# Kernel tuning notes

Hardware: AMD Instinct MI355X
Metric: run time of the kernel (lower is better)

Reference implementation:

```python
import jax, jax.numpy as jnp
import numpy as np

B, N, S, K = 8, 4096, 256, 128   # clouds, points/cloud, FPS samples (num_vote_test), neighbor cap
R = 0.2                           # ball-query radius
M = 45                            # FoldingNet grid side -> 45*45 = 2025 grid points


def _fps(pos):
    """Deterministic farthest point sampling of S points from pos [N,3] (start at index 0)."""
    n = pos.shape[0]
    big = jnp.finfo(pos.dtype).max

    def step(carry, _):
        mind, last = carry
        d = jnp.sum((pos - pos[last]) ** 2, axis=-1)
        mind = jnp.minimum(mind, d)
        nxt = jnp.argmax(mind).astype(jnp.int32)
        return (mind, nxt), nxt

    init = (jnp.full((n,), big, pos.dtype), jnp.int32(0))
    _, rest = jax.lax.scan(step, init, None, length=S - 1)
    return jnp.concatenate([jnp.zeros((1,), jnp.int32), rest])


def _forward(pos, Wt, bt, Wc1, bc1, Wc2, bc2, Wc3, bc3, We1, be1, We2, be2,
             Wf11, bf11, Wf12, bf12, Wf13, bf13, Wf21, bf21, Wf22, bf22, Wf23, bf23):
    lrelu = jax.nn.leaky_relu  # slope 0.01, matches torch LeakyReLU default
    # transformer: mlp([3,64]) -- BatchNorm at eval with default stats is identity
    x = lrelu(pos @ Wt + bt)                                  # [B,N,64]
    # FPS per cloud
    idx = jax.vmap(_fps)(pos)                                  # [B,S]
    new_pos = jnp.take_along_axis(pos, idx[..., None], axis=1)  # [B,S,3]
    # radius ball query: first K in-ball neighbors by index order (torch_cluster semantics)
    d2 = jnp.sum((new_pos[:, :, None, :] - pos[:, None, :, :]) ** 2, -1)  # [B,S,N]
    inball = d2 <= R * R
    keep = inball & (jnp.cumsum(inball, axis=-1) <= K)
    order = jnp.where(keep, jnp.arange(N)[None, None, :], N)
    nidx = jnp.sort(order, axis=-1)[..., :K]                   # [B,S,K]
    valid = nidx < N
    nsafe = jnp.minimum(nidx, N - 1)
    gather = jax.vmap(lambda a, i: a[i])
    xj = gather(x, nsafe)                                      # [B,S,K,64]
    pj = gather(pos, nsafe)                                    # [B,S,K,3]
    # PointConv: mlp(cat[x_j, pos_j - pos_i]) with max aggregation
    feat = jnp.concatenate([xj, pj - new_pos[:, :, None, :]], -1)  # [B,S,K,67]
    h = lrelu(feat @ Wc1 + bc1)
    h = lrelu(h @ Wc2 + bc2)
    h = lrelu(h @ Wc3 + bc3)                                   # [B,S,K,512]
    neg = jnp.finfo(h.dtype).min
    agg = jnp.max(jnp.where(valid[..., None], h, neg), axis=2)  # [B,S,512]
    # encoder mlp([515, 512, 2*bottleneck], last=True)
    e = lrelu(jnp.concatenate([agg, new_pos], -1) @ We1 + be1)
    e = e @ We2 + be2                                          # [B,S,2*bottleneck]
    mean, logvar = jnp.split(e, 2, axis=-1)
    std = jnp.exp(0.5 * logvar)
    # feature_selection (eval, rand=False): all S votes contribute; vote aggregation
    z = jnp.sum(mean / std, axis=1) / jnp.sum(1.0 / std, axis=1)  # [B,bottleneck]
    # FoldingNet decoder: 45x45 grid in [-0.3,0.3]^2, conv1x1 == last-dim linear
    g1 = np.linspace(-0.3, 0.3, M, dtype=np.float32)
    mg = np.meshgrid(g1, g1)
    grid = jnp.asarray(np.stack([mg[0].reshape(-1), mg[1].reshape(-1)], -1))  # [M*M,2]
    G = M * M
    code = jnp.broadcast_to(z[:, None, :], (z.shape[0], G, z.shape[1]))
    gb = jnp.broadcast_to(grid[None], (z.shape[0], G, 2))
    f = jnp.concatenate([code, gb], -1)                        # [B,G,bottleneck+2]
    f = jax.nn.relu(f @ Wf11 + bf11)
    f = jax.nn.relu(f @ Wf12 + bf12)
    f = f @ Wf13 + bf13                                        # [B,G,3]
    f2 = jnp.concatenate([code, f], -1)                        # [B,G,bottleneck+3]
    f2 = jax.nn.relu(f2 @ Wf21 + bf21)
    f2 = jax.nn.relu(f2 @ Wf22 + bf22)
    return f2 @ Wf23 + bf23                                    # [B,G,3]


_PARAM_SHAPES = [
    ("Wt", (3, 64)), ("bt", (64,)),
    ("Wc1", (67, 64)), ("bc1", (64,)),
    ("Wc2", (64, 128)), ("bc2", (128,)),
    ("Wc3", (128, 512)), ("bc3", (512,)),
    ("We1", (515, 512)), ("be1", (512,)),
    ("We2", (512, 2048)), ("be2", (2048,)),
    ("Wf11", (1026, 512)), ("bf11", (512,)),
    ("Wf12", (512, 512)), ("bf12", (512,)),
    ("Wf13", (512, 3)), ("bf13", (3,)),
    ("Wf21", (1027, 512)), ("bf21", (512,)),
    ("Wf22", (512, 512)), ("bf22", (512,)),
    ("Wf23", (512, 3)), ("bf23", (3,)),
]


def setup_inputs() -> dict:
    key = jax.random.key(0)
    inp = {"pos": jax.random.uniform(key, (B, N, 3), jnp.float32)}
    for i, (nm, sh) in enumerate(_PARAM_SHAPES):
        k = jax.random.fold_in(key, i + 1)
        fan_in = sh[0]
        inp[nm] = jax.random.normal(k, sh, jnp.float32) / np.sqrt(fan_in)
    return inp


def reference(pos, Wt, bt, Wc1, bc1, Wc2, bc2, Wc3, bc3, We1, be1, We2, be2,
              Wf11, bf11, Wf12, bf12, Wf13, bf13, Wf21, bf21, Wf22, bf22, Wf23, bf23):
    return _forward(pos, Wt, bt, Wc1, bc1, Wc2, bc2, Wc3, bc3, We1, be1, We2, be2,
                    Wf11, bf11, Wf12, bf12, Wf13, bf13, Wf21, bf21, Wf22, bf22, Wf23, bf23)
```

## Files before the change

kernel.cpp:

```cpp
#include <hip/hip_runtime.h>
#include <math.h>

#define BATCH 8
#define NPTS 4096
#define SSAMP 256
#define KNBR 128
#define GGRID 2025

typedef __attribute__((ext_vector_type(8))) short bf16x8;
typedef __attribute__((ext_vector_type(8))) unsigned short u16x8;
typedef __attribute__((ext_vector_type(4))) float f32x4;
#define MFMA16(a, b, c) __builtin_amdgcn_mfma_f32_16x16x32_bf16((a), (b), (c), 0, 0, 0)

__device__ __forceinline__ float lrelu01(float v) { return v > 0.f ? v : 0.01f * v; }
__device__ __forceinline__ unsigned short f2bf(float f) {
    unsigned u = __float_as_uint(f);
    unsigned r = (u + 0x7FFFu + ((u >> 16) & 1u)) >> 16;
    return (unsigned short)r;
}
__device__ __forceinline__ unsigned long long umax64(unsigned long long a, unsigned long long b) {
    return a > b ? a : b;
}
__device__ __forceinline__ void spin_ge(const int* p, int target) {
    while (__hip_atomic_load(p, __ATOMIC_RELAXED, __HIP_MEMORY_SCOPE_AGENT) < target)
        __builtin_amdgcn_s_sleep(16);
}
__device__ __forceinline__ float aload(const float* p) {
    return __hip_atomic_load((float*)p, __ATOMIC_RELAXED, __HIP_MEMORY_SCOPE_AGENT);
}
__device__ __forceinline__ void astore(float* p, float v) {
    __hip_atomic_store(p, v, __ATOMIC_RELAXED, __HIP_MEMORY_SCOPE_AGENT);
}

__global__ void preconv_kernel(const float* __restrict__ Wc1, const float* __restrict__ Wc2,
                               const float* __restrict__ Wc3, const float* __restrict__ We1,
                               const float* __restrict__ We2, const float* __restrict__ Wf12,
                               const float* __restrict__ Wf22,
                               unsigned short* __restrict__ W1T, unsigned short* __restrict__ W2T,
                               unsigned short* __restrict__ W3T, unsigned short* __restrict__ We1T,
                               unsigned short* __restrict__ We2T, unsigned short* __restrict__ Wf12T,
                               unsigned short* __restrict__ Wf22T) {
    int o = blockIdx.x * 256 + threadIdx.x;
    const int S1 = 6144, S2 = 8192, S3 = 65536, S4 = 294912, S5 = 1048576, S6 = 262144;
    if (o < S1) { int n = o / 96, k = o - n * 96; W1T[o] = f2bf(k < 67 ? Wc1[k * 64 + n] : 0.f); return; }
    o -= S1;
    if (o < S2) { int n = o >> 6, k = o & 63; W2T[o] = f2bf(Wc2[k * 128 + n]); return; }
    o -= S2;
    if (o < S3) { int n = o >> 7, k = o & 127; W3T[o] = f2bf(Wc3[k * 512 + n]); return; }
    o -= S3;
    if (o < S4) { int n = o / 576, k = o - n * 576; We1T[o] = f2bf(k < 515 ? We1[k * 512 + n] : 0.f); return; }
    o -= S4;
    if (o < S5) {
        int np = o >> 9, k = o & 511;
        int src = (np & 1) ? 1024 + (np >> 1) : (np >> 1);
        We2T[o] = f2bf(We2[(size_t)k * 2048 + src]);
        return;
    }
    o -= S5;
    if (o < S6) { int n = o >> 9, k = o & 511; Wf12T[o] = f2bf(Wf12[k * 512 + n]); return; }
    o -= S6;
    { int n = o >> 9, k = o & 511; Wf22T[o] = f2bf(Wf22[k * 512 + n]); }
}

__global__ void __launch_bounds__(256, 3) stage1_kernel(
    const float* __restrict__ pos, float* __restrict__ newpos, int* __restrict__ prog,
    const float* __restrict__ Wt, const float* __restrict__ bt,
    const unsigned short* __restrict__ W1T, const unsigned short* __restrict__ W2T,
    const unsigned short* __restrict__ W3T,
    const float* __restrict__ bc1, const float* __restrict__ bc2, const float* __restrict__ bc3,
    unsigned short* __restrict__ encin) {
    __shared__ __align__(16) unsigned char smem[53760];
    int blk = blockIdx.x, t = threadIdx.x;
    int wave = t >> 6, lane = t & 63;

    if (blk < 8) {
        float* pxs = (float*)smem;
        float* pys = (float*)(smem + 16384);
        float* pzs = (float*)(smem + 32768);
        float* npb = (float*)(smem + 49152);
        unsigned long long* rk = (unsigned long long*)(smem + 52224);
        int b = blk;
        const float* P = pos + (size_t)b * NPTS * 3;
        float* np = newpos + (size_t)b * SSAMP * 3;
        float px[16], py[16], pz[16], mind[16];
#pragma unroll
        for (int j = 0; j < 16; ++j) {
            int n = t + 256 * j;
            float X = P[n * 3 + 0], Y = P[n * 3 + 1], Z = P[n * 3 + 2];
            px[j] = X; py[j] = Y; pz[j] = Z;
            pxs[n] = X; pys[n] = Y; pzs[n] = Z;
            mind[j] = 3.402823466e+38f;
        }
        float cx = P[0], cy = P[1], cz = P[2];
        if (t == 0) { npb[0] = cx; npb[1] = cy; npb[2] = cz; }
        __syncthreads();
        for (int s = 1; s < SSAMP; ++s) {
            int p = s & 1;
            unsigned long long k[16];
#pragma unroll
            for (int j = 0; j < 16; ++j) {
                float dx = __fsub_rn(px[j], cx), dy = __fsub_rn(py[j], cy), dz = __fsub_rn(pz[j], cz);
                float d = __fadd_rn(__fadd_rn(__fmul_rn(dx, dx), __fmul_rn(dy, dy)), __fmul_rn(dz, dz));
                mind[j] = fminf(mind[j], d);
                k[j] = ((unsigned long long)__float_as_uint(mind[j]) << 32)
                     | (unsigned)~(unsigned)(t + 256 * j);
            }
#pragma unroll
            for (int st = 8; st > 0; st >>= 1)
#pragma unroll
                for (int j = 0; j < st; ++j) k[j] = umax64(k[j], k[j + st]);
            unsigned long long key = k[0];
            {
                unsigned long long a = __shfl_xor(key, 1, 64);
                unsigned long long b2 = __shfl_xor(key, 2, 64);
                unsigned long long c = __shfl_xor(key, 3, 64);
                key = umax64(umax64(key, a), umax64(b2, c));
                a = __shfl_xor(key, 4, 64);
                b2 = __shfl_xor(key, 8, 64);
                c = __shfl_xor(key, 12, 64);
                key = umax64(umax64(key, a), umax64(b2, c));
                a = __shfl_xor(key, 16, 64);
                b2 = __shfl_xor(key, 32, 64);
                c = __shfl_xor(key, 48, 64);
                key = umax64(umax64(key, a), umax64(b2, c));
            }
            if (lane == 0) rk[p * 4 + wave] = key;
            __syncthreads();
            unsigned long long k0 = rk[p * 4 + 0], k1 = rk[p * 4 + 1];
            unsigned long long k2 = rk[p * 4 + 2], k3 = rk[p * 4 + 3];
            unsigned long long bk = umax64(umax64(k0, k1), umax64(k2, k3));
            int nx = (int)(~(unsigned)(bk & 0xFFFFFFFFull));
            cx = pxs[nx]; cy = pys[nx]; cz = pzs[nx];
            if (t == 0) {
                npb[s * 3 + 0] = cx;
                npb[s * 3 + 1] = cy;
                npb[s * 3 + 2] = cz;
            }
            if ((s & 7) == 7) {
                if (t < 24) astore(&np[(s - 7) * 3 + t], npb[(s - 7) * 3 + t]);
                if (t == 0 && s >= 15)
                    __hip_atomic_store(&prog[b], s - 8, __ATOMIC_RELAXED, __HIP_MEMORY_SCOPE_AGENT);
            }
        }
        __syncthreads();
        if (t == 0)
            __hip_atomic_store(&prog[b], 255, __ATOMIC_RELAXED, __HIP_MEMORY_SCOPE_AGENT);
        return;
    }

    unsigned short* featl = (unsigned short*)smem;
    unsigned short* h2    = (unsigned short*)smem;
    unsigned short* h1    = (unsigned short*)(smem + 34816);
    float* mred = (float*)(smem + 34816);
    int*   vld  = (int*)(smem + 53248);
    int*   wl   = (int*)smem;
    int*   cnt  = (int*)(smem + 2048);
    float* wtb  = (float*)(smem + 26624);

    int cons = blk - 8;
    int s = cons >> 3, b = cons & 7;
    int bs = b * 256 + s;
    int quad = lane >> 4, l16 = lane & 15;

    if (t == 0) spin_ge(&prog[b], s);
    __syncthreads();
    float q0 = aload(&newpos[(size_t)bs * 3 + 0]);
    float q1 = aload(&newpos[(size_t)bs * 3 + 1]);
    float q2 = aload(&newpos[(size_t)bs * 3 + 2]);

    const float* P = pos + (size_t)b * NPTS * 3;
    {
        int base = 0;
        for (int c = 0; c < 16 && base < KNBR; ++c) {
            int n = wave * 1024 + c * 64 + lane;
            float dx = __fsub_rn(P[n * 3 + 0], q0);
            float dy = __fsub_rn(P[n * 3 + 1], q1);
            float dz = __fsub_rn(P[n * 3 + 2], q2);
            float d2 = __fadd_rn(__fadd_rn(__fmul_rn(dx, dx), __fmul_rn(dy, dy)), __fmul_rn(dz, dz));
            bool in = (d2 <= 0.04f);
            unsigned long long mask = __ballot(in);
            if (in) {
                int p = base + __popcll(mask & ((1ull << lane) - 1ull));
                if (p < KNBR) wl[wave * 128 + p] = n;
            }
            base += __popcll(mask);
        }
        if (lane == 0) cnt[wave] = base < KNBR ? base : KNBR;
    }
    __syncthreads();
    {
        int c0 = cnt[0], c1 = cnt[1], c2 = cnt[2], c3 = cnt[3];
        if (t < 128) {
            int idx = -1, r = t;
            if (r < c0) idx = wl[r];
            else {
                r -= c0;
                if (r < c1) idx = wl[128 + r];
                else {
                    r -= c1;
                    if (r < c2) idx = wl[256 + r];
                    else { r -= c2; if (r < c3) idx = wl[384 + r]; }
                }
            }
            vld[t] = idx;
        }
        if (t < 192) wtb[t] = Wt[t];
        else wtb[t] = bt[t - 192];
    }
    __syncthreads();

    int vbits = 0;
#pragma unroll
    for (int i = 0; i < 2; ++i)
#pragma unroll
        for (int reg = 0; reg < 4; ++reg)
            if (vld[(2 * wave + i) * 16 + quad * 4 + reg] >= 0) vbits |= 1 << (i * 4 + reg);

    {
        int sr = t >> 1, sh = t & 1;
        int n = vld[sr];
        int ns = n < 0 ? 0 : n;
        const float* pp = pos + ((size_t)b * NPTS + ns) * 3;
        float p0 = pp[0], p1 = pp[1], p2 = pp[2];
        unsigned short* frow = &featl[sr * 104];
        u16x8 z8 = {0, 0, 0, 0, 0, 0, 0, 0};
        if (n >= 0) {
#pragma unroll
            for (int g = 0; g < 4; ++g) {
                u16x8 v8;
#pragma unroll
                for (int e = 0; e < 8; ++e) {
                    int c = sh * 32 + g * 8 + e;
                    float v = fmaf(p2, wtb[128 + c], fmaf(p1, wtb[64 + c], fmaf(p0, wtb[c], wtb[192 + c])));
                    v8[e] = (unsigned short)f2bf(lrelu01(v));
                }
                *(u16x8*)&frow[sh * 32 + g * 8] = v8;
            }
        } else {
#pragma unroll
            for (int g = 0; g < 4; ++g) *(u16x8*)&frow[sh * 32 + g * 8] = z8;
        }
        if (sh == 1) {
            u16x8 dv = z8;
            if (n >= 0) {
                dv[0] = (unsigned short)f2bf(__fsub_rn(p0, q0));
                dv[1] = (unsigned short)f2bf(__fsub_rn(p1, q1));
                dv[2] = (unsigned short)f2bf(__fsub_rn(p2, q2));
            }
            *(u16x8*)&frow[64] = dv;
            *(u16x8*)&frow[72] = z8;
            *(u16x8*)&frow[80] = z8;
            *(u16x8*)&frow[88] = z8;
        }
    }
    __syncthreads();

    {
        f32x4 acc[2][4];
#pragma unroll
        for (int i = 0; i < 2; ++i)
#pragma unroll
            for (int nt = 0; nt < 4; ++nt) acc[i][nt] = (f32x4){0.f, 0.f, 0.f, 0.f};
#pragma unroll
        for (int ks = 0; ks < 3; ++ks) {
            bf16x8 afr[2];
#pragma unroll
            for (int i = 0; i < 2; ++i)
                afr[i] = *(const bf16x8*)&featl[((2 * wave + i) * 16 + l16) * 104 + ks * 32 + quad * 8];
#pragma unroll
            for (int nt = 0; nt < 4; ++nt) {
                bf16x8 bfr = *(const bf16x8*)(W1T + (nt * 16 + l16) * 96 + ks * 32 + quad * 8);
                acc[0][nt] = MFMA16(afr[0], bfr, acc[0][nt]);
                acc[1][nt] = MFMA16(afr[1], bfr, acc[1][nt]);
            }
        }
#pragma unroll
        for (int i = 0; i < 2; ++i)
#pragma unroll
            for (int nt = 0; nt < 4; ++nt) {
                int col = nt * 16 + l16;
                float bias = bc1[col];
#pragma unroll
                for (int reg = 0; reg < 4; ++reg) {
                    int row = (2 * wave + i) * 16 + quad * 4 + reg;
                    h1[row * 72 + col] = f2bf(lrelu01(acc[i][nt][reg] + bias));
                }
            }
    }
    __syncthreads();

    {
        f32x4 acc[2][8];
#pragma unroll
        for (int i = 0; i < 2; ++i)
#pragma unroll
            for (int nt = 0; nt < 8; ++nt) acc[i][nt] = (f32x4){0.f, 0.f, 0.f, 0.f};
#pragma unroll
        for (int ks = 0; ks < 2; ++ks) {
            bf16x8 afr[2];
#pragma unroll
            for (int i = 0; i < 2; ++i)
                afr[i] = *(const bf16x8*)&h1[((2 * wave + i) * 16 + l16) * 72 + ks * 32 + quad * 8];
#pragma unroll
            for (int nt = 0; nt < 8; ++nt) {
                bf16x8 bfr = *(const bf16x8*)(W2T + (nt * 16 + l16) * 64 + ks * 32 + quad * 8);
                acc[0][nt] = MFMA16(afr[0], bfr, acc[0][nt]);
                acc[1][nt] = MFMA16(afr[1], bfr, acc[1][nt]);
            }
        }
        __syncthreads();
#pragma unroll
        for (int i = 0; i < 2; ++i)
#pragma unroll
            for (int nt = 0; nt < 8; ++nt) {
                int col = nt * 16 + l16;
                float bias = bc2[col];
#pragma unroll
                for (int reg = 0; reg < 4; ++reg) {
                    int row = (2 * wave + i) * 16 + quad * 4 + reg;
                    h2[row * 136 + col] = f2bf(lrelu01(acc[i][nt][reg] + bias));
                }
            }
    }
    __syncthreads();

    for (int c3 = 0; c3 < 4; ++c3) {
        f32x4 acc[2][8];
#pragma unroll
        for (int i = 0; i < 2; ++i)
#pragma unroll
            for (int nt = 0; nt < 8; ++nt) acc[i][nt] = (f32x4){0.f, 0.f, 0.f, 0.f};
#pragma unroll
        for (int ks = 0; ks < 4; ++ks) {
            bf16x8 afr[2];
#pragma unroll
            for (int i = 0; i < 2; ++i)
                afr[i] = *(const bf16x8*)&h2[((2 * wave + i) * 16 + l16) * 136 + ks * 32 + quad * 8];
#pragma unroll
            for (int nt = 0; nt < 8; ++nt) {
                bf16x8 bfr = *(const bf16x8*)(W3T + ((size_t)((c3 * 8 + nt) * 16 + l16)) * 128 + ks * 32 + quad * 8);
                acc[0][nt] = MFMA16(afr[0], bfr, acc[0][nt]);
                acc[1][nt] = MFMA16(afr[1], bfr, acc[1][nt]);
            }
        }
#pragma unroll
        for (int nt = 0; nt < 8; ++nt) {
            float vmax = -3.402823466e+38f;
#pragma unroll
            for (int i = 0; i < 2; ++i)
#pragma unroll
                for (int reg = 0; reg < 4; ++reg)
                    if (vbits & (1 << (i * 4 + reg))) vmax = fmaxf(vmax, acc[i][nt][reg]);
            vmax = fmaxf(vmax, __shfl_xor(vmax, 16));
            vmax = fmaxf(vmax, __shfl_xor(vmax, 32));
            if (lane < 16) mred[wave * 512 + (c3 * 8 + nt) * 16 + l16] = vmax;
        }
    }
    __syncthreads();
    unsigned short* erow = encin + (size_t)bs * 576;
    for (int c = t; c < 576; c += 256) {
        unsigned short v;
        if (c < 512) {
            float m4 = fmaxf(fmaxf(mred[c], mred[512 + c]), fmaxf(mred[1024 + c], mred[1536 + c]));
            v = f2bf(lrelu01(m4 + bc3[c]));
        } else if (c < 515) {
            v = f2bf(c == 512 ? q0 : (c == 513 ? q1 : q2));
        } else v = 0;
        erow[c] = v;
    }
}

__global__ void __launch_bounds__(256, 2) tail_kernel(
    const unsigned short* __restrict__ encinh, const unsigned short* __restrict__ We1T,
    const float* __restrict__ be1, unsigned short* __restrict__ e1h,
    const unsigned short* __restrict__ We2T, const float* __restrict__ be2,
    float* __restrict__ zacc, int* __restrict__ cnts,
    const float* __restrict__ Wf11, const float* __restrict__ bf11,
    const float* __restrict__ Wf21, const float* __restrict__ bf21,
    float* __restrict__ u1, float* __restrict__ u2,
    const unsigned short* __restrict__ Wf12T, const float* __restrict__ bf12,
    const float* __restrict__ Wf13, const float* __restrict__ bf13,
    const unsigned short* __restrict__ Wf22T, const float* __restrict__ bf22,
    const float* __restrict__ Wf23, const float* __restrict__ bf23,
    float* __restrict__ pts, float* __restrict__ outv) {
    __shared__ __align__(16) unsigned char smem[40960];
    int blk = blockIdx.x, t = threadIdx.x;
    int wave = t >> 6, lane = t & 63, quad = lane >> 4, l16 = lane & 15;

    if (blk < 320) {
        unsigned short* As = (unsigned short*)smem;
        bool is_e1 = blk < 64;
        int rb, cb;
        const unsigned short* A;
        const unsigned short* BT;
        int Ka;
        if (is_e1) { rb = blk >> 2; cb = blk & 3; A = encinh; BT = We1T; Ka = 576; }
        else {
            int j = blk - 64; rb = j >> 4; cb = j & 15; A = e1h; BT = We2T; Ka = 512;
            if (t == 0) spin_ge(&cnts[rb], 4);
            __syncthreads();
            __threadfence();
        }
        int row0 = rb * 128, col0 = cb * 128;
        f32x4 acc[2][8];
#pragma unroll
        for (int i = 0; i < 2; ++i)
#pragma unroll
            for (int nt = 0; nt < 8; ++nt) acc[i][nt] = (f32x4){0.f, 0.f, 0.f, 0.f};
        int nk = Ka >> 6;
        int sr = t >> 1, sh = t & 1;
        const unsigned short* Arow = A + (size_t)(row0 + sr) * Ka + sh * 32;
        for (int ks = 0; ks < nk; ++ks) {
            u16x8 av[4];
#pragma unroll
            for (int j = 0; j < 4; ++j) av[j] = *(const u16x8*)(Arow + ks * 64 + j * 8);
            __syncthreads();
#pragma unroll
            for (int j = 0; j < 4; ++j) *(u16x8*)&As[sr * 72 + sh * 32 + j * 8] = av[j];
            __syncthreads();
#pragma unroll
            for (int ks2 = 0; ks2 < 2; ++ks2) {
                bf16x8 afr0 = *(const bf16x8*)&As[((2 * wave) * 16 + l16) * 72 + ks2 * 32 + quad * 8];
                bf16x8 afr1 = *(const bf16x8*)&As[((2 * wave + 1) * 16 + l16) * 72 + ks2 * 32 + quad * 8];
#pragma unroll
                for (int nt = 0; nt < 8; ++nt) {
                    bf16x8 bfr = *(const bf16x8*)(BT + (size_t)(col0 + nt * 16 + l16) * Ka + ks * 64 + ks2 * 32 + quad * 8);
                    acc[0][nt] = MFMA16(afr0, bfr, acc[0][nt]);
                    acc[1][nt] = MFMA16(afr1, bfr, acc[1][nt]);
                }
            }
        }
        if (is_e1) {
#pragma unroll
            for (int i = 0; i < 2; ++i)
#pragma unroll
                for (int nt = 0; nt < 8; ++nt) {
                    int col = col0 + nt * 16 + l16;
                    float bv = be1[col];
#pragma unroll
                    for (int reg = 0; reg < 4; ++reg) {
                        int row = row0 + (2 * wave + i) * 16 + quad * 4 + reg;
                        e1h[(size_t)row * 512 + col] = f2bf(lrelu01(acc[i][nt][reg] + bv));
                    }
                }
            __syncthreads();
            if (t == 0) { __threadfence(); atomicAdd(&cnts[rb], 1); }
        } else {
            int b = row0 >> 8;
#pragma unroll
            for (int nt = 0; nt < 8; ++nt) {
                int colp = col0 + nt * 16 + l16;
                int c2 = colp >> 1;
                int srcc = (colp & 1) ? 1024 + c2 : c2;
                float bv = be2[srcc];
                float num = 0.f, den = 0.f;
#pragma unroll
                for (int i = 0; i < 2; ++i)
#pragma unroll
                    for (int reg = 0; reg < 4; ++reg) {
                        float val = acc[i][nt][reg] + bv;
                        float par = __shfl_xor(val, 1, 64);
                        float d = expf(-0.5f * par);
                        num += val * d;
                        den += d;
                    }
                num += __shfl_xor(num, 16, 64); den += __shfl_xor(den, 16, 64);
                num += __shfl_xor(num, 32, 64); den += __shfl_xor(den, 32, 64);
                if (quad == 0 && !(l16 & 1)) {
                    atomicAdd(&zacc[((b << 10) + c2) * 2 + 0], num);
                    atomicAdd(&zacc[((b << 10) + c2) * 2 + 1], den);
                }
            }
            __syncthreads();
            if (t == 0) atomicAdd(&cnts[16], 1);
        }
        return;
    }

    if (blk < 336) {
        float* zt = (float*)smem;
        float* red = (float*)(smem + 32768);
        int j = blk - 320;
        int dec = j >> 3, cb = j & 7;
        const float* W = dec ? Wf21 : Wf11;
        const float* bias = dec ? bf21 : bf11;
        float* u = dec ? u2 : u1;
        if (t == 0) spin_ge(&cnts[16], 256);
        __syncthreads();
#pragma unroll
        for (int i = 0; i < 32; ++i) {
            int o = t + i * 256;
            float num = aload(&zacc[o * 2 + 0]);
            float den = aload(&zacc[o * 2 + 1]);
            zt[(o & 1023) * 8 + (o >> 10)] = num / den;
        }
        __syncthreads();
        int c64 = t & 63, kc = t >> 6;
        int co = cb * 64 + c64;
        float acc[8];
#pragma unroll
        for (int r = 0; r < 8; ++r) acc[r] = 0.f;
        for (int i = 0; i < 256; ++i) {
            int ci = kc * 256 + i;
            float w = W[(size_t)ci * 512 + co];
            const float4* zp = (const float4*)&zt[ci * 8];
            float4 z0 = zp[0], z1 = zp[1];
            acc[0] = fmaf(z0.x, w, acc[0]); acc[1] = fmaf(z0.y, w, acc[1]);
            acc[2] = fmaf(z0.z, w, acc[2]); acc[3] = fmaf(z0.w, w, acc[3]);
            acc[4] = fmaf(z1.x, w, acc[4]); acc[5] = fmaf(z1.y, w, acc[5]);
            acc[6] = fmaf(z1.z, w, acc[6]); acc[7] = fmaf(z1.w, w, acc[7]);
        }
#pragma unroll
        for (int r = 0; r < 8; ++r) red[(kc * 64 + c64) * 8 + r] = acc[r];
        __syncthreads();
        if (kc == 0) {
#pragma unroll
            for (int r = 0; r < 8; ++r) {
                float v = red[(0 * 64 + c64) * 8 + r] + red[(1 * 64 + c64) * 8 + r]
                        + red[(2 * 64 + c64) * 8 + r] + red[(3 * 64 + c64) * 8 + r] + bias[co];
                astore(&u[r * 512 + co], v);
            }
        }
        __syncthreads();
        if (t == 0) atomicAdd(&cnts[17 + dec], 1);
        return;
    }

    {
        unsigned short* As = (unsigned short*)smem;
        float* sW = (float*)(smem + 18432);
        float* sU = (float*)(smem + 24576);
        float* sP = (float*)(smem + 28672);
        float* sB = (float*)(smem + 30208);
        float* sRC = (float*)(smem + 30720);
        int dec = blk < 844 ? 0 : 1;
        int idx0 = blk - (dec ? 844 : 336);
        int j = idx0 >> 2, cc = idx0 & 3;
        const float* u = dec ? u2 : u1;
        const float* Wfold = dec ? Wf21 : Wf11;
        int nExtra = dec ? 3 : 2;
        const unsigned short* WT = dec ? Wf22T : Wf12T;
        const float* bmid = dec ? bf22 : bf12;
        const float* wout = dec ? Wf23 : Wf13;
        const float* bout = dec ? bf23 : bf13;
        float* ov = dec ? outv : pts;
        int row0 = j * 128, col0 = cc * 128;
        int b0 = row0 / 2025;

        if (t == 0) {
            spin_ge(&cnts[17 + dec], 8);
            if (dec) spin_ge(&cnts[20 + j], 4);
        }
        __syncthreads();

        for (int idx = t; idx < 1536; idx += 256) {
            int r = idx >> 9, c = idx & 511;
            sW[r * 512 + c] = (r < nExtra) ? Wfold[(size_t)(1024 + r) * 512 + c] : 0.f;
        }
        for (int idx = t; idx < 1024; idx += 256) {
            int rb = idx >> 9;
            int bb = b0 + rb; if (bb > 7) bb = 7;
            sU[rb * 512 + (idx & 511)] = aload(&u[bb * 512 + (idx & 511)]);
        }
        for (int idx = t; idx < 384; idx += 256) sP[idx] = wout[col0 * 3 + idx];
        if (t < 128) sB[t] = bmid[col0 + t];
        if (t < 128) {
            int rg = row0 + t; if (rg > 16199) rg = 16199;
            int b = rg / 2025, g = rg - b * 2025;
            if (dec == 0) {
                int i = g / 45, jj = g - i * 45;
                sRC[t * 4 + 0] = (jj == 44) ? 0.3f : (float)(-0.3 + jj * (0.6 / 44.0));
                sRC[t * 4 + 1] = (i == 44) ? 0.3f : (float)(-0.3 + i * (0.6 / 44.0));
                sRC[t * 4 + 2] = 0.f;
            } else {
                sRC[t * 4 + 0] = aload(&pts[rg * 3 + 0]);
                sRC[t * 4 + 1] = aload(&pts[rg * 3 + 1]);
                sRC[t * 4 + 2] = aload(&pts[rg * 3 + 2]);
            }
            sRC[t * 4 + 3] = __int_as_float(b - b0);
        }
        __syncthreads();

        float proj[2][4][3];
#pragma unroll
        for (int i = 0; i < 2; ++i)
#pragma unroll
            for (int r = 0; r < 4; ++r) { proj[i][r][0] = 0.f; proj[i][r][1] = 0.f; proj[i][r][2] = 0.f; }

        int sr = t >> 1, sh = t & 1;
        float4 rc = *(const float4*)&sRC[sr * 4];
        int ubi = __float_as_int(rc.w);
        const float* up = sU + ubi * 512;
        f32x4 acc[2][8];
#pragma unroll
        for (int i = 0; i < 2; ++i)
#pragma unroll
            for (int nt = 0; nt < 8; ++nt) acc[i][nt] = (f32x4){0.f, 0.f, 0.f, 0.f};
        for (int ks = 0; ks < 8; ++ks) {
            __syncthreads();
            {
                int cbase = ks * 64 + sh * 32;
                const float4* w0p = (const float4*)&sW[cbase];
                const float4* w1p = (const float4*)&sW[512 + cbase];
                const float4* w2p = (const float4*)&sW[1024 + cbase];
                const float4* uup = (const float4*)&up[cbase];
#pragma unroll
                for (int g4 = 0; g4 < 8; ++g4) {
                    float4 w0 = w0p[g4], w1 = w1p[g4], w2 = w2p[g4], uu = uup[g4];
                    float v0 = fmaf(rc.z, w2.x, fmaf(rc.y, w1.x, fmaf(rc.x, w0.x, uu.x)));
                    float v1 = fmaf(rc.z, w2.y, fmaf(rc.y, w1.y, fmaf(rc.x, w0.y, uu.y)));
                    float v2 = fmaf(rc.z, w2.z, fmaf(rc.y, w1.z, fmaf(rc.x, w0.z, uu.z)));
                    float v3 = fmaf(rc.z, w2.w, fmaf(rc.y, w1.w, fmaf(rc.x, w0.w, uu.w)));
                    uint2 pk;
                    pk.x = (unsigned)f2bf(fmaxf(v0, 0.f)) | ((unsigned)f2bf(fmaxf(v1, 0.f)) << 16);
                    pk.y = (unsigned)f2bf(fmaxf(v2, 0.f)) | ((unsigned)f2bf(fmaxf(v3, 0.f)) << 16);
                    *(uint2*)&As[sr * 72 + sh * 32 + g4 * 4] = pk;
                }
            }
            __syncthreads();
#pragma unroll
            for (int ks2 = 0; ks2 < 2; ++ks2) {
                bf16x8 afr0 = *(const bf16x8*)&As[((2 * wave) * 16 + l16) * 72 + ks2 * 32 + quad * 8];
                bf16x8 afr1 = *(const bf16x8*)&As[((2 * wave + 1) * 16 + l16) * 72 + ks2 * 32 + quad * 8];
#pragma unroll
                for (int nt = 0; nt < 8; ++nt) {
                    bf16x8 bfr = *(const bf16x8*)(WT + (size_t)(col0 + nt * 16 + l16) * 512 + ks * 64 + ks2 * 32 + quad * 8);
                    acc[0][nt] = MFMA16(afr0, bfr, acc[0][nt]);
                    acc[1][nt] = MFMA16(afr1, bfr, acc[1][nt]);
                }
            }
        }
#pragma unroll
        for (int i = 0; i < 2; ++i)
#pragma unroll
            for (int nt = 0; nt < 8; ++nt) {
                int lc = nt * 16 + l16;
                float bv = sB[lc];
                float w0 = sP[lc * 3 + 0], w1 = sP[lc * 3 + 1], w2 = sP[lc * 3 + 2];
#pragma unroll
                for (int reg = 0; reg < 4; ++reg) {
                    float h = fmaxf(acc[i][nt][reg] + bv, 0.f);
                    proj[i][reg][0] = fmaf(h, w0, proj[i][reg][0]);
                    proj[i][reg][1] = fmaf(h, w1, proj[i][reg][1]);
                    proj[i][reg][2] = fmaf(h, w2, proj[i][reg][2]);
                }
            }
        float o0 = (cc == 0) ? bout[0] : 0.f;
        float o1 = (cc == 0) ? bout[1] : 0.f;
        float o2 = (cc == 0) ? bout[2] : 0.f;
#pragma unroll
        for (int i = 0; i < 2; ++i)
#pragma unroll
            for (int reg = 0; reg < 4; ++reg) {
                float p0 = proj[i][reg][0], p1 = proj[i][reg][1], p2 = proj[i][reg][2];
#pragma unroll
                for (int m = 1; m < 16; m <<= 1) {
                    p0 += __shfl_xor(p0, m, 64);
                    p1 += __shfl_xor(p1, m, 64);
                    p2 += __shfl_xor(p2, m, 64);
                }
                if (l16 == 0) {
                    int row = row0 + (2 * wave + i) * 16 + quad * 4 + reg;
                    if (row < 16200) {
                        atomicAdd(&ov[row * 3 + 0], p0 + o0);
                        atomicAdd(&ov[row * 3 + 1], p1 + o1);
                        atomicAdd(&ov[row * 3 + 2], p2 + o2);
                    }
                }
            }
        if (dec == 0) {
            __syncthreads();
            if (t == 0) atomicAdd(&cnts[20 + j], 1);
        }
    }
}

extern "C" void kernel_launch(void* const* d_in, const int* in_sizes, int n_in,
                              void* d_out, int out_size, void* d_ws, size_t ws_size,
                              hipStream_t stream) {
    const float* pos  = (const float*)d_in[0];
    const float* Wt   = (const float*)d_in[1];
    const float* bt   = (const float*)d_in[2];
    const float* Wc1  = (const float*)d_in[3];
    const float* bc1  = (const float*)d_in[4];
    const float* Wc2  = (const float*)d_in[5];
    const float* bc2  = (const float*)d_in[6];
    const float* Wc3  = (const float*)d_in[7];
    const float* bc3  = (const float*)d_in[8];
    const float* We1  = (const float*)d_in[9];
    const float* be1  = (const float*)d_in[10];
    const float* We2  = (const float*)d_in[11];
    const float* be2  = (const float*)d_in[12];
    const float* Wf11 = (const float*)d_in[13];
    const float* bf11 = (const float*)d_in[14];
    const float* Wf12 = (const float*)d_in[15];
    const float* bf12 = (const float*)d_in[16];
    const float* Wf13 = (const float*)d_in[17];
    const float* bf13 = (const float*)d_in[18];
    const float* Wf21 = (const float*)d_in[19];
    const float* bf21 = (const float*)d_in[20];
    const float* Wf22 = (const float*)d_in[21];
    const float* bf22 = (const float*)d_in[22];
    const float* Wf23 = (const float*)d_in[23];
    const float* bf23 = (const float*)d_in[24];
    float* out = (float*)d_out;

    float* wsf = (float*)d_ws;
    size_t off = 0;
    unsigned short* encinh= (unsigned short*)(wsf + off); off += 589824;
    unsigned short* e1h   = (unsigned short*)(wsf + off); off += 524288;
    float* zacc = wsf + off; off += 16384;
    float* u1   = wsf + off; off += 4096;
    float* u2   = wsf + off; off += 4096;
    float* pts  = wsf + off; off += 48600;
    float* newp = wsf + off; off += 6144;
    int*   prog = (int*)(wsf + off); off += 16;
    int*   cnts = (int*)(wsf + off); off += 256;
    unsigned short* W1T   = (unsigned short*)(wsf + off); off += 3072;
    unsigned short* W2T   = (unsigned short*)(wsf + off); off += 4096;
    unsigned short* W3T   = (unsigned short*)(wsf + off); off += 32768;
    unsigned short* We1T  = (unsigned short*)(wsf + off); off += 147456;
    unsigned short* We2T  = (unsigned short*)(wsf + off); off += 524288;
    unsigned short* Wf12T = (unsigned short*)(wsf + off); off += 131072;
    unsigned short* Wf22T = (unsigned short*)(wsf + off); off += 131072;

    hipMemsetAsync(prog, 0xFF, 64, stream);
    hipMemsetAsync(cnts, 0x00, 1024, stream);
    hipMemsetAsync(zacc, 0x00, 16384 * 4, stream);
    hipMemsetAsync(pts, 0x00, 48600 * 4, stream);
    hipMemsetAsync(out, 0x00, (size_t)out_size * 4, stream);
    preconv_kernel<<<7608, 256, 0, stream>>>(Wc1, Wc2, Wc3, We1, We2, Wf12, Wf22,
                                             W1T, W2T, W3T, We1T, We2T, Wf12T, Wf22T);
    stage1_kernel<<<2056, 256, 0, stream>>>(pos, newp, prog, Wt, bt, W1T, W2T, W3T,
                                            bc1, bc2, bc3, encinh);
    tail_kernel<<<1352, 256, 0, stream>>>(encinh, We1T, be1, e1h, We2T, be2, zacc, cnts,
                                          Wf11, bf11, Wf21, bf21, u1, u2,
                                          Wf12T, bf12, Wf13, bf13,
                                          Wf22T, bf22, Wf23, bf23, pts, out);
}
```

Before: 607.4 us.

## Move large weight conversions into tail kernel and overlap with dependent GEMM stages

The single preconversion kernel is split. Only the small stage1 and We1 weights are converted before stage1, using a compact grid with 8 elements per thread. The large We2/Wf12/Wf22 bf16 transposes move into extra leading blocks of the tail kernel, which signal completion through counters, and the e2 and fold blocks spin on those counters before reading. Fold blocks now stage their independent data before waiting, and stage1 consumers poll with a longer sleep to reduce contention on the FPS progress flags. The aim is to take the weight conversion off the critical path by overlapping it with earlier work, at the cost of more spin-waiting and a larger tail grid.

```diff
diff --git a/kernel.cpp b/kernel.cpp
--- a/kernel.cpp
+++ b/kernel.cpp
@@ -25,6 +25,10 @@
     while (__hip_atomic_load(p, __ATOMIC_RELAXED, __HIP_MEMORY_SCOPE_AGENT) < target)
         __builtin_amdgcn_s_sleep(16);
 }
+__device__ __forceinline__ void spin_ge_slow(const int* p, int target) {
+    while (__hip_atomic_load(p, __ATOMIC_RELAXED, __HIP_MEMORY_SCOPE_AGENT) < target)
+        __builtin_amdgcn_s_sleep(64);
+}
 __device__ __forceinline__ float aload(const float* p) {
     return __hip_atomic_load((float*)p, __ATOMIC_RELAXED, __HIP_MEMORY_SCOPE_AGENT);
 }
@@ -32,34 +36,24 @@
     __hip_atomic_store(p, v, __ATOMIC_RELAXED, __HIP_MEMORY_SCOPE_AGENT);
 }
 
-__global__ void preconv_kernel(const float* __restrict__ Wc1, const float* __restrict__ Wc2,
-                               const float* __restrict__ Wc3, const float* __restrict__ We1,
-                               const float* __restrict__ We2, const float* __restrict__ Wf12,
-                               const float* __restrict__ Wf22,
-                               unsigned short* __restrict__ W1T, unsigned short* __restrict__ W2T,
-                               unsigned short* __restrict__ W3T, unsigned short* __restrict__ We1T,
-                               unsigned short* __restrict__ We2T, unsigned short* __restrict__ Wf12T,
-                               unsigned short* __restrict__ Wf22T) {
+__global__ void preconv1_kernel(const float* __restrict__ Wc1, const float* __restrict__ Wc2,
+                                const float* __restrict__ Wc3, const float* __restrict__ We1,
+                                unsigned short* __restrict__ W1T, unsigned short* __restrict__ W2T,
+                                unsigned short* __restrict__ W3T, unsigned short* __restrict__ We1T) {
     int o = blockIdx.x * 256 + threadIdx.x;
-    const int S1 = 6144, S2 = 8192, S3 = 65536, S4 = 294912, S5 = 1048576, S6 = 262144;
-    if (o < S1) { int n = o / 96, k = o - n * 96; W1T[o] = f2bf(k < 67 ? Wc1[k * 64 + n] : 0.f); return; }
-    o -= S1;
-    if (o < S2) { int n = o >> 6, k = o & 63; W2T[o] = f2bf(Wc2[k * 128 + n]); return; }
-    o -= S2;
-    if (o < S3) { int n = o >> 7, k = o & 127; W3T[o] = f2bf(Wc3[k * 512 + n]); return; }
-    o -= S3;
-    if (o < S4) { int n = o / 576, k = o - n * 576; We1T[o] = f2bf(k < 515 ? We1[k * 512 + n] : 0.f); return; }
-    o -= S4;
-    if (o < S5) {
-        int np = o >> 9, k = o & 511;
-        int src = (np & 1) ? 1024 + (np >> 1) : (np >> 1);
-        We2T[o] = f2bf(We2[(size_t)k * 2048 + src]);
-        return;
-    }
-    o -= S5;
-    if (o < S6) { int n = o >> 9, k = o & 511; Wf12T[o] = f2bf(Wf12[k * 512 + n]); return; }
-    o -= S6;
-    { int n = o >> 9, k = o & 511; Wf22T[o] = f2bf(Wf22[k * 512 + n]); }
+    const int S1 = 6144, S2 = 8192, S3 = 65536;
+#pragma unroll
+    for (int j = 0; j < 8; ++j) {
+        int q = o + j * 47104;
+        if (q >= 374784) continue;
+        if (q < S1) { int n = q / 96, k = q - n * 96; W1T[q] = f2bf(k < 67 ? Wc1[k * 64 + n] : 0.f); continue; }
+        q -= S1;
+        if (q < S2) { int n = q >> 6, k = q & 63; W2T[q] = f2bf(Wc2[k * 128 + n]); continue; }
+        q -= S2;
+        if (q < S3) { int n = q >> 7, k = q & 127; W3T[q] = f2bf(Wc3[k * 512 + n]); continue; }
+        q -= S3;
+        { int n = q / 576, k = q - n * 576; We1T[q] = f2bf(k < 515 ? We1[k * 512 + n] : 0.f); }
+    }
 }
 
 __global__ void __launch_bounds__(256, 3) stage1_kernel(
@@ -162,7 +156,7 @@
     int bs = b * 256 + s;
     int quad = lane >> 4, l16 = lane & 15;
 
-    if (t == 0) spin_ge(&prog[b], s);
+    if (t == 0) spin_ge_slow(&prog[b], s);
     __syncthreads();
     float q0 = aload(&newpos[(size_t)bs * 3 + 0]);
     float q1 = aload(&newpos[(size_t)bs * 3 + 1]);
@@ -371,33 +365,60 @@
 }
 
 __global__ void __launch_bounds__(256, 2) tail_kernel(
+    const float* __restrict__ We2, const float* __restrict__ Wf12, const float* __restrict__ Wf22,
+    unsigned short* __restrict__ We2T, unsigned short* __restrict__ Wf12T,
+    unsigned short* __restrict__ Wf22T,
     const unsigned short* __restrict__ encinh, const unsigned short* __restrict__ We1T,
     const float* __restrict__ be1, unsigned short* __restrict__ e1h,
-    const unsigned short* __restrict__ We2T, const float* __restrict__ be2,
+    const float* __restrict__ be2,
     float* __restrict__ zacc, int* __restrict__ cnts,
     const float* __restrict__ Wf11, const float* __restrict__ bf11,
     const float* __restrict__ Wf21, const float* __restrict__ bf21,
     float* __restrict__ u1, float* __restrict__ u2,
-    const unsigned short* __restrict__ Wf12T, const float* __restrict__ bf12,
+    const float* __restrict__ bf12,
     const float* __restrict__ Wf13, const float* __restrict__ bf13,
-    const unsigned short* __restrict__ Wf22T, const float* __restrict__ bf22,
+    const float* __restrict__ bf22,
     const float* __restrict__ Wf23, const float* __restrict__ bf23,
     float* __restrict__ pts, float* __restrict__ outv) {
     __shared__ __align__(16) unsigned char smem[40960];
     int blk = blockIdx.x, t = threadIdx.x;
     int wave = t >> 6, lane = t & 63, quad = lane >> 4, l16 = lane & 15;
 
-    if (blk < 320) {
+    if (blk < 768) {
+        const int S5 = 1048576, S6 = 262144;
+#pragma unroll
+        for (int j = 0; j < 8; ++j) {
+            int q = blk * 2048 + t + j * 256;
+            if (q < S5) {
+                int np2 = q >> 9, k = q & 511;
+                int src = (np2 & 1) ? 1024 + (np2 >> 1) : (np2 >> 1);
+                We2T[q] = f2bf(We2[(size_t)k * 2048 + src]);
+                continue;
+            }
+            q -= S5;
+            if (q < S6) { int n = q >> 9, k = q & 511; Wf12T[q] = f2bf(Wf12[k * 512 + n]); continue; }
+            q -= S6;
+            { int n = q >> 9, k = q & 511; Wf22T[q] = f2bf(Wf22[k * 512 + n]); }
+        }
+        __syncthreads();
+        if (t == 0) {
+            __threadfence();
+            atomicAdd(&cnts[blk < 512 ? 148 : 149], 1);
+        }
+        return;
+    }
+
+    if (blk < 1088) {
         unsigned short* As = (unsigned short*)smem;
-        bool is_e1 = blk < 64;
+        bool is_e1 = blk < 832;
         int rb, cb;
         const unsigned short* A;
         const unsigned short* BT;
         int Ka;
-        if (is_e1) { rb = blk >> 2; cb = blk & 3; A = encinh; BT = We1T; Ka = 576; }
+        if (is_e1) { int j = blk - 768; rb = j >> 2; cb = j & 3; A = encinh; BT = We1T; Ka = 576; }
         else {
-            int j = blk - 64; rb = j >> 4; cb = j & 15; A = e1h; BT = We2T; Ka = 512;
-            if (t == 0) spin_ge(&cnts[rb], 4);
+            int j = blk - 832; rb = j >> 4; cb = j & 15; A = e1h; BT = We2T; Ka = 512;
+            if (t == 0) { spin_ge(&cnts[148], 512); spin_ge(&cnts[rb], 4); }
             __syncthreads();
             __threadfence();
         }
@@ -477,10 +498,10 @@
         return;
     }
 
-    if (blk < 336) {
+    if (blk < 1104) {
         float* zt = (float*)smem;
         float* red = (float*)(smem + 32768);
-        int j = blk - 320;
+        int j = blk - 1088;
         int dec = j >> 3, cb = j & 7;
         const float* W = dec ? Wf21 : Wf11;
         const float* bias = dec ? bf21 : bf11;
@@ -533,8 +554,8 @@
         float* sP = (float*)(smem + 28672);
         float* sB = (float*)(smem + 30208);
         float* sRC = (float*)(smem + 30720);
-        int dec = blk < 844 ? 0 : 1;
-        int idx0 = blk - (dec ? 844 : 336);
+        int dec = blk < 1612 ? 0 : 1;
+        int idx0 = blk - (dec ? 1612 : 1104);
         int j = idx0 >> 2, cc = idx0 & 3;
         const float* u = dec ? u2 : u1;
         const float* Wfold = dec ? Wf21 : Wf11;
@@ -547,36 +568,41 @@
         int row0 = j * 128, col0 = cc * 128;
         int b0 = row0 / 2025;
 
-        if (t == 0) {
-            spin_ge(&cnts[17 + dec], 8);
-            if (dec) spin_ge(&cnts[20 + j], 4);
-        }
-        __syncthreads();
-
         for (int idx = t; idx < 1536; idx += 256) {
             int r = idx >> 9, c = idx & 511;
             sW[r * 512 + c] = (r < nExtra) ? Wfold[(size_t)(1024 + r) * 512 + c] : 0.f;
         }
+        for (int idx = t; idx < 384; idx += 256) sP[idx] = wout[col0 * 3 + idx];
+        if (t < 128) sB[t] = bmid[col0 + t];
+        if (dec == 0 && t < 128) {
+            int rg = row0 + t; if (rg > 16199) rg = 16199;
+            int b = rg / 2025, g = rg - b * 2025;
+            int i = g / 45, jj = g - i * 45;
+            sRC[t * 4 + 0] = (jj == 44) ? 0.3f : (float)(-0.3 + jj * (0.6 / 44.0));
+            sRC[t * 4 + 1] = (i == 44) ? 0.3f : (float)(-0.3 + i * (0.6 / 44.0));
+            sRC[t * 4 + 2] = 0.f;
+            sRC[t * 4 + 3] = __int_as_float(b - b0);
+        }
+
+        if (t == 0) {
+            spin_ge(&cnts[149], 256);
+            spin_ge(&cnts[17 + dec], 8);
+            if (dec) spin_ge(&cnts[20 + j], 4);
+        }
+        __syncthreads();
+        __threadfence();
+
         for (int idx = t; idx < 1024; idx += 256) {
             int rb = idx >> 9;
             int bb = b0 + rb; if (bb > 7) bb = 7;
             sU[rb * 512 + (idx & 511)] = aload(&u[bb * 512 + (idx & 511)]);
         }
-        for (int idx = t; idx < 384; idx += 256) sP[idx] = wout[col0 * 3 + idx];
-        if (t < 128) sB[t] = bmid[col0 + t];
-        if (t < 128) {
+        if (dec == 1 && t < 128) {
             int rg = row0 + t; if (rg > 16199) rg = 16199;
-            int b = rg / 2025, g = rg - b * 2025;
-            if (dec == 0) {
-                int i = g / 45, jj = g - i * 45;
-                sRC[t * 4 + 0] = (jj == 44) ? 0.3f : (float)(-0.3 + jj * (0.6 / 44.0));
-                sRC[t * 4 + 1] = (i == 44) ? 0.3f : (float)(-0.3 + i * (0.6 / 44.0));
-                sRC[t * 4 + 2] = 0.f;
-            } else {
-                sRC[t * 4 + 0] = aload(&pts[rg * 3 + 0]);
-                sRC[t * 4 + 1] = aload(&pts[rg * 3 + 1]);
-                sRC[t * 4 + 2] = aload(&pts[rg * 3 + 2]);
-            }
+            int b = rg / 2025;
+            sRC[t * 4 + 0] = aload(&pts[rg * 3 + 0]);
+            sRC[t * 4 + 1] = aload(&pts[rg * 3 + 1]);
+            sRC[t * 4 + 2] = aload(&pts[rg * 3 + 2]);
             sRC[t * 4 + 3] = __int_as_float(b - b0);
         }
         __syncthreads();
@@ -729,12 +755,11 @@
     hipMemsetAsync(zacc, 0x00, 16384 * 4, stream);
     hipMemsetAsync(pts, 0x00, 48600 * 4, stream);
     hipMemsetAsync(out, 0x00, (size_t)out_size * 4, stream);
-    preconv_kernel<<<7608, 256, 0, stream>>>(Wc1, Wc2, Wc3, We1, We2, Wf12, Wf22,
-                                             W1T, W2T, W3T, We1T, We2T, Wf12T, Wf22T);
+    preconv1_kernel<<<184, 256, 0, stream>>>(Wc1, Wc2, Wc3, We1, W1T, W2T, W3T, We1T);
     stage1_kernel<<<2056, 256, 0, stream>>>(pos, newp, prog, Wt, bt, W1T, W2T, W3T,
                                             bc1, bc2, bc3, encinh);
-    tail_kernel<<<1352, 256, 0, stream>>>(encinh, We1T, be1, e1h, We2T, be2, zacc, cnts,
+    tail_kernel<<<2120, 256, 0, stream>>>(We2, Wf12, Wf22, We2T, Wf12T, Wf22T,
+                                          encinh, We1T, be1, e1h, be2, zacc, cnts,
                                           Wf11, bf11, Wf21, bf21, u1, u2,
-                                          Wf12T, bf12, Wf13, bf13,
-                                          Wf22T, bf22, Wf23, bf23, pts, out);
-}
+                                          bf12, Wf13, bf13, bf22, Wf23, bf23, pts, out);
+}
```

After: 781.0 us. 1.29x slower.
